# Optimization experiments

Hardware: AMD Instinct MI355X
Metric: run time of the kernel (lower is better)

Reference implementation:

```python
import jax, jax.numpy as jnp
import numpy as np

D_MODEL, D_K, D_V, D_H, SEQ = 1024, 64, 64, 16, 4096


def setup_inputs() -> dict:
    key = jax.random.key(0)
    ks = jax.random.split(key, 16)
    s = lambda fan_in: 1.0 / np.sqrt(fan_in)
    return {
        "X": jax.random.normal(ks[0], (SEQ, D_MODEL), jnp.float32),
        # shared Q/K/V projections (nn.Linear stores weight as [out, in])
        "Wq": jax.random.uniform(ks[1], (D_K, D_MODEL), jnp.float32, -s(D_MODEL), s(D_MODEL)),
        "bq": jax.random.uniform(ks[2], (D_K,), jnp.float32, -s(D_MODEL), s(D_MODEL)),
        "Wk": jax.random.uniform(ks[3], (D_K, D_MODEL), jnp.float32, -s(D_MODEL), s(D_MODEL)),
        "bk": jax.random.uniform(ks[4], (D_K,), jnp.float32, -s(D_MODEL), s(D_MODEL)),
        "Wv": jax.random.uniform(ks[5], (D_V, D_MODEL), jnp.float32, -s(D_MODEL), s(D_MODEL)),
        "bv": jax.random.uniform(ks[6], (D_V,), jnp.float32, -s(D_MODEL), s(D_MODEL)),
        # per-head linears stacked along head axis
        "Whq": jax.random.uniform(ks[7], (D_H, D_K, D_K), jnp.float32, -s(D_K), s(D_K)),
        "bhq": jax.random.uniform(ks[8], (D_H, D_K), jnp.float32, -s(D_K), s(D_K)),
        "Whk": jax.random.uniform(ks[9], (D_H, D_K, D_K), jnp.float32, -s(D_K), s(D_K)),
        "bhk": jax.random.uniform(ks[10], (D_H, D_K), jnp.float32, -s(D_K), s(D_K)),
        "Whv": jax.random.uniform(ks[11], (D_H, D_V, D_V), jnp.float32, -s(D_V), s(D_V)),
        "bhv": jax.random.uniform(ks[12], (D_H, D_V), jnp.float32, -s(D_V), s(D_V)),
        # final projection: d_h*d_v -> d_model
        "Wo": jax.random.uniform(ks[13], (D_MODEL, D_H * D_V), jnp.float32, -s(D_H * D_V), s(D_H * D_V)),
        "bo": jax.random.uniform(ks[14], (D_MODEL,), jnp.float32, -s(D_H * D_V), s(D_H * D_V)),
    }


def reference(X, Wq, bq, Wk, bk, Wv, bv, Whq, bhq, Whk, bhk, Whv, bhv, Wo, bo):
    # shared projections: [T, d_k] / [T, d_v]
    Q = X @ Wq.T + bq
    K = X @ Wk.T + bk
    V = X @ Wv.T + bv
    # per-head linears, all heads at once: [H, T, d_k]
    qh = jnp.einsum("tk,hjk->htj", Q, Whq) + bhq[:, None, :]
    kh = jnp.einsum("tk,hjk->htj", K, Whk) + bhk[:, None, :]
    vh = jnp.einsum("tv,hjv->htj", V, Whv) + bhv[:, None, :]
    # scaled dot-product attention per head: [H, T, T]
    scale = 1.0 / jnp.sqrt(jnp.asarray(Q.shape[-1], X.dtype))
    attn = jax.nn.softmax(jnp.einsum("htk,hsk->hts", qh, kh) * scale, axis=-1)
    rep = jnp.einsum("hts,hsv->htv", attn, vh)  # [H, T, d_v]
    # hstack heads -> [T, H*d_v], then final projection
    concat = rep.transpose(1, 0, 2).reshape(X.shape[0], -1)
    return concat @ Wo.T + bo
```

## Files before the change

### kernel.cpp

```cpp
#include <hip/hip_runtime.h>

#define T 4096
#define DM 1024
#define DK 64
#define H 16

typedef short s8 __attribute__((ext_vector_type(8)));
typedef float f4 __attribute__((ext_vector_type(4)));
typedef float f16v __attribute__((ext_vector_type(16)));
typedef unsigned short us4 __attribute__((ext_vector_type(4)));
typedef unsigned u32x2 __attribute__((ext_vector_type(2)));
typedef unsigned u32x4 __attribute__((ext_vector_type(4)));
typedef __bf16 bf2 __attribute__((ext_vector_type(2)));

#define MFMA16(a,b,c) __builtin_amdgcn_mfma_f32_16x16x32_bf16((a),(b),(c),0,0,0)
#define MFMA32(a,b,c) __builtin_amdgcn_mfma_f32_32x32x16_bf16((a),(b),(c),0,0,0)
#define SCALE_Q 0.18033688011112042f

__device__ __forceinline__ unsigned short f2bf(float x){
  __bf16 b = (__bf16)x;
  return __builtin_bit_cast(unsigned short, b);
}
__device__ __forceinline__ unsigned pk2(float a, float b){
  bf2 v; v[0] = (__bf16)a; v[1] = (__bf16)b;
  return __builtin_bit_cast(unsigned, v);
}

__device__ __forceinline__ void gload16(const void* g, void* lds){
  __builtin_amdgcn_global_load_lds((const __attribute__((address_space(1))) unsigned int*)g,
                                   (__attribute__((address_space(3))) unsigned int*)lds,
                                   16, 0, 0);
}

__device__ __forceinline__ void swp(unsigned X, unsigned Y, unsigned &E, unsigned &O){
#if __has_builtin(__builtin_amdgcn_permlane32_swap)
  auto a = __builtin_amdgcn_permlane32_swap(X, Y, false, false);
  E = a[0]; O = a[1];
#else
  int l = threadIdx.x & 63;
  unsigned sx = __builtin_amdgcn_ds_bpermute(((l & 31) << 2), X);
  unsigned sy = __builtin_amdgcn_ds_bpermute(((l & 31) << 2), Y);
  unsigned hx = __builtin_amdgcn_ds_bpermute((((l & 31) + 32) << 2), X);
  unsigned hy = __builtin_amdgcn_ds_bpermute((((l & 31) + 32) << 2), Y);
  E = (l < 32) ? sx : sy;
  O = (l < 32) ? hx : hy;
#endif
}

__global__ void cvt_bf16(const float* __restrict__ in, unsigned short* __restrict__ out, int n4){
  int i = blockIdx.x * blockDim.x + threadIdx.x;
  if (i >= n4) return;
  float4 v = reinterpret_cast<const float4*>(in)[i];
  us4 o;
  o[0] = f2bf(v.x); o[1] = f2bf(v.y); o[2] = f2bf(v.z); o[3] = f2bf(v.w);
  reinterpret_cast<us4*>(out)[i] = o;
}

#define N_WOB (DM * DM / 4)
#define N_W3  (64 * DM / 4)
#define N_WH  (16 * 64 * 64 / 4)
__global__ __launch_bounds__(256) void prep_all(
    const float* __restrict__ Wo,
    const float* __restrict__ Wq, const float* __restrict__ Wk, const float* __restrict__ Wv,
    const float* __restrict__ Whq, const float* __restrict__ Whk, const float* __restrict__ Whv,
    const float* __restrict__ bq, const float* __restrict__ bk, const float* __restrict__ bv,
    const float* __restrict__ bhq, const float* __restrict__ bhk, const float* __restrict__ bhv,
    unsigned short* __restrict__ Wob, unsigned short* __restrict__ W3b,
    unsigned short* __restrict__ Whb, float* __restrict__ beff){
  int idx = blockIdx.x * 256 + threadIdx.x;
  if (idx < N_WOB){
    float4 v = reinterpret_cast<const float4*>(Wo)[idx];
    us4 o; o[0]=f2bf(v.x); o[1]=f2bf(v.y); o[2]=f2bf(v.z); o[3]=f2bf(v.w);
    reinterpret_cast<us4*>(Wob)[idx] = o;
    return;
  }
  idx -= N_WOB;
  if (idx < 3 * N_W3){
    int seg = idx / N_W3, i = idx - seg * N_W3;
    const float* src = (seg == 0) ? Wq : ((seg == 1) ? Wk : Wv);
    float4 v = reinterpret_cast<const float4*>(src)[i];
    us4 o; o[0]=f2bf(v.x); o[1]=f2bf(v.y); o[2]=f2bf(v.z); o[3]=f2bf(v.w);
    reinterpret_cast<us4*>(W3b)[seg * N_W3 + i] = o;
    return;
  }
  idx -= 3 * N_W3;
  if (idx < 3 * N_WH){
    int seg = idx / N_WH, i = idx - seg * N_WH;
    const float* src = (seg == 0) ? Whq : ((seg == 1) ? Whk : Whv);
    float s = (seg == 0) ? SCALE_Q : 1.0f;
    float4 v = reinterpret_cast<const float4*>(src)[i];
    us4 o; o[0]=f2bf(v.x*s); o[1]=f2bf(v.y*s); o[2]=f2bf(v.z*s); o[3]=f2bf(v.w*s);
    reinterpret_cast<us4*>(Whb)[seg * N_WH + i] = o;
    return;
  }
  idx -= 3 * N_WH;
  if (idx < 3072){
    int seg = idx >> 10, j = idx & 1023;
    const float* Wh = (seg == 0) ? Whq : ((seg == 1) ? Whk : Whv);
    const float* b  = (seg == 0) ? bq  : ((seg == 1) ? bk  : bv);
    const float* bh = (seg == 0) ? bhq : ((seg == 1) ? bhk : bhv);
    float s = (seg == 0) ? SCALE_Q : 1.0f;
    const float* wr = Wh + j * 64;
    float acc = 0.f;
    #pragma unroll 8
    for (int k = 0; k < 64; ++k) acc += wr[k] * b[k];
    beff[idx] = (acc + bh[j]) * s;
  }
}

template<int MODE, int BM, int BN, int NT>
__global__ __launch_bounds__(256) void gemmX(const unsigned short* __restrict__ A,
                       const unsigned short* __restrict__ B,
                       const float* __restrict__ bias,
                       unsigned short* __restrict__ q_out,
                       unsigned short* __restrict__ k_out,
                       unsigned short* __restrict__ v_out,
                       float* __restrict__ f_out){
  __shared__ __align__(16) short la[2][BM * 64];
  __shared__ __align__(16) short lb[2][BN * 64];
  const int tid = threadIdx.x;
  const int wv = tid >> 6, l = tid & 63;
  const int lr = l & 15, lh = l >> 4;
  const int wr = wv >> 1, wc = wv & 1;
  const int tm = blockIdx.x / NT, tn = blockIdx.x % NT;
  const int t0 = tm * BM, o0 = tn * BN;
  constexpr int MF = BM / 32;
  constexpr int NF = BN / 32;
  constexpr int ACH = BM / 32;
  constexpr int BCH = BN / 32;
  constexpr int LAB = BM * 128;
  constexpr int LBB = BN * 128;

  f4 acc[MF][NF];
  #pragma unroll
  for (int i = 0; i < MF; ++i)
    #pragma unroll
    for (int j = 0; j < NF; ++j) acc[i][j] = (f4){0.f, 0.f, 0.f, 0.f};

  const int srow = tid >> 3;
  const int scs  = (tid & 7) ^ (srow & 7);
  const unsigned short* ap = A + (size_t)(t0 + srow) * DM + scs * 8;
  const unsigned short* bp = B + (size_t)(o0 + srow) * DM + scs * 8;
  char* ad = (char*)&la[0][0] + tid * 16;
  char* bd = (char*)&lb[0][0] + tid * 16;

  auto stage = [&](int BUF){
    #pragma unroll
    for (int i = 0; i < ACH; ++i)
      gload16(ap + (size_t)i * 32 * DM, ad + BUF * LAB + i * 4096);
    #pragma unroll
    for (int i = 0; i < BCH; ++i)
      gload16(bp + (size_t)i * 32 * DM, bd + BUF * LBB + i * 4096);
    ap += 64; bp += 64;
  };

  const int asw0 = (lh ^ (lr & 7)) * 16, asw1 = ((lh ^ 4) ^ (lr & 7)) * 16;
  const char* aB0 = (const char*)&la[0][0] + (wr * (BM / 2) + lr) * 128 + asw0;
  const char* aB1 = (const char*)&la[0][0] + (wr * (BM / 2) + lr) * 128 + asw1;
  const char* bB0 = (const char*)&lb[0][0] + (wc * (BN / 2) + lr) * 128 + asw0;
  const char* bB1 = (const char*)&lb[0][0] + (wc * (BN / 2) + lr) * 128 + asw1;

  auto step = [&](int BUF, bool dostage){
    if (dostage) stage(BUF ^ 1);
    s8 af[MF][2], bfr[NF][2];
    #pragma unroll
    for (int mf = 0; mf < MF; ++mf){
      af[mf][0] = *(const s8*)(aB0 + BUF * LAB + mf * 2048);
      af[mf][1] = *(const s8*)(aB1 + BUF * LAB + mf * 2048);
    }
    #pragma unroll
    for (int nf = 0; nf < NF; ++nf){
      bfr[nf][0] = *(const s8*)(bB0 + BUF * LBB + nf * 2048);
      bfr[nf][1] = *(const s8*)(bB1 + BUF * LBB + nf * 2048);
    }
    __builtin_amdgcn_s_setprio(1);
    #pragma unroll
    for (int mf = 0; mf < MF; ++mf)
      #pragma unroll
      for (int nf = 0; nf < NF; ++nf){
        acc[mf][nf] = MFMA16(af[mf][0], bfr[nf][0], acc[mf][nf]);
        acc[mf][nf] = MFMA16(af[mf][1], bfr[nf][1], acc[mf][nf]);
      }
    __builtin_amdgcn_s_setprio(0);
    __syncthreads();
  };

  stage(0);
  __syncthreads();
  #pragma unroll 1
  for (int t2 = 0; t2 < 8; ++t2){
    step(0, true);
    step(1, t2 < 7);
  }

  #pragma unroll
  for (int nf = 0; nf < NF; ++nf){
    int o = o0 + wc * (BN / 2) + nf * 16 + lr;
    float bs = (MODE == 4) ? 0.f : bias[o];
    int sel = o >> 6, oc = o & 63;
    unsigned short* yo = (sel == 0) ? q_out : ((sel == 1) ? k_out : v_out);
    #pragma unroll
    for (int mf = 0; mf < MF; ++mf)
      #pragma unroll
      for (int r = 0; r < 4; ++r){
        int t = t0 + wr * (BM / 2) + mf * 16 + lh * 4 + r;
        float v = acc[mf][nf][r] + bs;
        if (MODE == 2) f_out[(size_t)t * DM + o] = v;
        else           yo[(size_t)t * 64 + oc] = f2bf(v);
      }
  }
}

__global__ __launch_bounds__(256) void gemm_heads(const unsigned short* __restrict__ Yq,
                        const unsigned short* __restrict__ Yk,
                        const unsigned short* __restrict__ Yv,
                        const unsigned short* __restrict__ Whb,
                        const float* __restrict__ beff,
                        unsigned short* __restrict__ qhb,
                        unsigned short* __restrict__ khb,
                        unsigned short* __restrict__ vtb){
  const int tid = threadIdx.x;
  const int wv = tid >> 6, l = tid & 63;
  const int lr = l & 15, lh = l >> 4;
  const int rem = blockIdx.x % 48, tb = blockIdx.x / 48;
  const int kind = rem >> 4, h = rem & 15;
  const unsigned short* Y = (kind == 0) ? Yq : ((kind == 1) ? Yk : Yv);
  const unsigned short* B = Whb + (size_t)rem * 4096;
  const int t0 = tb * 256 + wv * 64;

  s8 wf[4][2], yf[4][2];
  #pragma unroll
  for (int nf = 0; nf < 4; ++nf)
    #pragma unroll
    for (int hf = 0; hf < 2; ++hf)
      wf[nf][hf] = *reinterpret_cast<const s8*>(B + (size_t)(nf * 16 + lr) * 64 + hf * 32 + lh * 8);
  #pragma unroll
  for (int mf = 0; mf < 4; ++mf)
    #pragma unroll
    for (int hf = 0; hf < 2; ++hf)
      yf[mf][hf] = *reinterpret_cast<const s8*>(Y + (size_t)(t0 + mf * 16 + lr) * 64 + hf * 32 + lh * 8);

  f4 acc[4][4];
  #pragma unroll
  for (int i = 0; i < 4; ++i)
    #pragma unroll
    for (int j = 0; j < 4; ++j) acc[i][j] = (f4){0.f, 0.f, 0.f, 0.f};

  if (kind < 2){
    #pragma unroll
    for (int mf = 0; mf < 4; ++mf)
      #pragma unroll
      for (int nf = 0; nf < 4; ++nf){
        acc[mf][nf] = MFMA16(yf[mf][0], wf[nf][0], acc[mf][nf]);
        acc[mf][nf] = MFMA16(yf[mf][1], wf[nf][1], acc[mf][nf]);
      }
    unsigned short* out = (kind == 0) ? qhb : khb;
    #pragma unroll
    for (int nf = 0; nf < 4; ++nf){
      int j = nf * 16 + lr;
      float bs = beff[rem * 64 + j];
      #pragma unroll
      for (int mf = 0; mf < 4; ++mf)
        #pragma unroll
        for (int r = 0; r < 4; ++r){
          int t = t0 + mf * 16 + lh * 4 + r;
          out[((size_t)h * T + t) * DK + j] = f2bf(acc[mf][nf][r] + bs);
        }
    }
  } else {
    #pragma unroll
    for (int nf = 0; nf < 4; ++nf)
      #pragma unroll
      for (int mf = 0; mf < 4; ++mf){
        acc[nf][mf] = MFMA16(wf[nf][0], yf[mf][0], acc[nf][mf]);
        acc[nf][mf] = MFMA16(wf[nf][1], yf[mf][1], acc[nf][mf]);
      }
    #pragma unroll
    for (int nf = 0; nf < 4; ++nf){
      float4 bsv = *reinterpret_cast<const float4*>(beff + rem * 64 + nf * 16 + lh * 4);
      #pragma unroll
      for (int r = 0; r < 4; ++r){
        int j = nf * 16 + lh * 4 + r;
        float bs = (r == 0) ? bsv.x : ((r == 1) ? bsv.y : ((r == 2) ? bsv.z : bsv.w));
        #pragma unroll
        for (int mf = 0; mf < 4; ++mf){
          int t = t0 + mf * 16 + lr;
          vtb[((size_t)h * DK + j) * T + t] = f2bf(acc[nf][mf][r] + bs);
        }
      }
    }
  }
}

__global__ __launch_bounds__(256) void attn_fwd(const unsigned short* __restrict__ qh,
                         const unsigned short* __restrict__ kh,
                         const unsigned short* __restrict__ vt,
                         unsigned short* __restrict__ cat){
  __shared__ __align__(16) char ldsb[2][16384];
  const int tid = threadIdx.x;
  const int wv = tid >> 6, l = tid & 63;
  const int l31 = l & 31, h5 = l >> 5, l7 = l & 7;
  const int h = blockIdx.x >> 5, qblk = blockIdx.x & 31;
  const int Q0w = qblk * 128 + wv * 32;

  s8 qf[4];
  #pragma unroll
  for (int kk = 0; kk < 4; ++kk)
    qf[kk] = *reinterpret_cast<const s8*>(
        qh + ((size_t)h * T + Q0w + l31) * DK + kk * 16 + h5 * 8);

  float ls = 0.f;
  f16v oa0, oa1;
  #pragma unroll
  for (int i = 0; i < 16; ++i){ oa0[i] = 0.f; oa1[i] = 0.f; }

  const int srow = tid >> 3;
  const int scs  = (tid & 7) ^ (srow & 7);
  const unsigned short* kp = kh + (size_t)h * T * DK + srow * DK + scs * 8;
  const unsigned short* vp = vt + (size_t)h * DK * T + srow * T + scs * 8;
  char* sd = &ldsb[0][0] + tid * 16;

  auto stage = [&](int BUF){
    gload16(kp,           sd + BUF * 16384);
    gload16(kp + 32 * DK, sd + BUF * 16384 + 4096);
    gload16(vp,           sd + BUF * 16384 + 8192);
    gload16(vp + 32 * T,  sd + BUF * 16384 + 12288);
    kp += 64 * DK; vp += 64;
  };

  const char* ba[2][4];
  #pragma unroll
  for (int t2 = 0; t2 < 2; ++t2)
    #pragma unroll
    for (int kk = 0; kk < 4; ++kk)
      ba[t2][kk] = &ldsb[0][0] + (t2 * 32 + l31) * 128 + ((((kk << 1) | h5) ^ l7) << 4);

  auto step = [&](int BUF, bool dostage){
    if (dostage) stage(BUF ^ 1);
    s8 kf0[4], kf1[4];
    #pragma unroll
    for (int kk = 0; kk < 4; ++kk){
      kf0[kk] = *(const s8*)(ba[0][kk] + BUF * 16384);
      kf1[kk] = *(const s8*)(ba[1][kk] + BUF * 16384);
    }
    f16v sc0, sc1;
    #pragma unroll
    for (int i = 0; i < 16; ++i){ sc0[i] = 0.f; sc1[i] = 0.f; }
    __builtin_amdgcn_s_setprio(1);
    #pragma unroll
    for (int kk = 0; kk < 4; ++kk) sc0 = MFMA32(kf0[kk], qf[kk], sc0);
    #pragma unroll
    for (int kk = 0; kk < 4; ++kk) sc1 = MFMA32(kf1[kk], qf[kk], sc1);
    __builtin_amdgcn_s_setprio(0);
    s8 vf0[4], vf1[4];
    #pragma unroll
    for (int p = 0; p < 4; ++p){
      vf0[p] = *(const s8*)(ba[0][p] + BUF * 16384 + 8192);
      vf1[p] = *(const s8*)(ba[1][p] + BUF * 16384 + 8192);
    }
    float p0[16], p1[16];
    #pragma unroll
    for (int i = 0; i < 16; ++i){
      p0[i] = __builtin_amdgcn_exp2f(sc0[i]);
      p1[i] = __builtin_amdgcn_exp2f(sc1[i]);
    }
    float r0 = (p0[0]+p0[1]) + (p0[2]+p0[3]);
    float r1 = (p0[4]+p0[5]) + (p0[6]+p0[7]);
    float r2 = (p0[8]+p0[9]) + (p0[10]+p0[11]);
    float r3 = (p0[12]+p0[13]) + (p0[14]+p0[15]);
    float r4 = (p1[0]+p1[1]) + (p1[2]+p1[3]);
    float r5 = (p1[4]+p1[5]) + (p1[6]+p1[7]);
    float r6 = (p1[8]+p1[9]) + (p1[10]+p1[11]);
    float r7 = (p1[12]+p1[13]) + (p1[14]+p1[15]);
    ls += ((r0+r1)+(r2+r3)) + ((r4+r5)+(r6+r7));
    unsigned a0 = pk2(p0[0],p0[1]),  a1 = pk2(p0[2],p0[3]);
    unsigned a2 = pk2(p0[4],p0[5]),  a3 = pk2(p0[6],p0[7]);
    unsigned a4 = pk2(p0[8],p0[9]),  a5 = pk2(p0[10],p0[11]);
    unsigned a6 = pk2(p0[12],p0[13]), a7 = pk2(p0[14],p0[15]);
    unsigned b0 = pk2(p1[0],p1[1]),  b1 = pk2(p1[2],p1[3]);
    unsigned b2 = pk2(p1[4],p1[5]),  b3 = pk2(p1[6],p1[7]);
    unsigned b4 = pk2(p1[8],p1[9]),  b5 = pk2(p1[10],p1[11]);
    unsigned b6 = pk2(p1[12],p1[13]), b7 = pk2(p1[14],p1[15]);
    unsigned e0,o0, e1,o1, e2,o2, e3,o3, e4,o4, e5,o5, e6,o6, e7,o7;
    swp(a0, a2, e0, o0);  swp(a1, a3, e1, o1);
    swp(a4, a6, e2, o2);  swp(a5, a7, e3, o3);
    swp(b0, b2, e4, o4);  swp(b1, b3, e5, o5);
    swp(b4, b6, e6, o6);  swp(b5, b7, e7, o7);
    u32x4 pu0 = {e0, e1, o0, o1};
    u32x4 pu1 = {e2, e3, o2, o3};
    u32x4 pu2 = {e4, e5, o4, o5};
    u32x4 pu3 = {e6, e7, o6, o7};
    s8 pa0 = __builtin_bit_cast(s8, pu0);
    s8 pa1 = __builtin_bit_cast(s8, pu1);
    s8 pa2 = __builtin_bit_cast(s8, pu2);
    s8 pa3 = __builtin_bit_cast(s8, pu3);
    __builtin_amdgcn_s_setprio(1);
    oa0 = MFMA32(vf0[0], pa0, oa0);
    oa0 = MFMA32(vf0[1], pa1, oa0);
    oa0 = MFMA32(vf0[2], pa2, oa0);
    oa0 = MFMA32(vf0[3], pa3, oa0);
    oa1 = MFMA32(vf1[0], pa0, oa1);
    oa1 = MFMA32(vf1[1], pa1, oa1);
    oa1 = MFMA32(vf1[2], pa2, oa1);
    oa1 = MFMA32(vf1[3], pa3, oa1);
    __builtin_amdgcn_s_setprio(0);
    __syncthreads();
  };

  stage(0);
  __syncthreads();
  #pragma unroll 1
  for (int it = 0; it < 32; ++it){
    step(0, true);
    step(1, it < 31);
  }

  float lq = ls + __shfl_xor(ls, 32);
  float inv = 1.f / lq;
  const int t = Q0w + l31;
  unsigned short* crow = cat + (size_t)t * DM + h * DK;
  #pragma unroll
  for (int g = 0; g < 4; ++g){
    u32x2 w0, w1;
    w0[0] = pk2(oa0[g*4+0] * inv, oa0[g*4+1] * inv);
    w0[1] = pk2(oa0[g*4+2] * inv, oa0[g*4+3] * inv);
    w1[0] = pk2(oa1[g*4+0] * inv, oa1[g*4+1] * inv);
    w1[1] = pk2(oa1[g*4+2] * inv, oa1[g*4+3] * inv);
    *reinterpret_cast<u32x2*>(crow + g * 8 + h5 * 4)      = w0;
    *reinterpret_cast<u32x2*>(crow + 32 + g * 8 + h5 * 4) = w1;
  }
}

extern "C" void kernel_launch(void* const* d_in, const int* in_sizes, int n_in,
                              void* d_out, int out_size, void* d_ws, size_t ws_size,
                              hipStream_t stream){
  const float* X   = (const float*)d_in[0];
  const float* Wq  = (const float*)d_in[1];
  const float* bq  = (const float*)d_in[2];
  const float* Wk  = (const float*)d_in[3];
  const float* bk  = (const float*)d_in[4];
  const float* Wv  = (const float*)d_in[5];
  const float* bv  = (const float*)d_in[6];
  const float* Whq = (const float*)d_in[7];
  const float* bhq = (const float*)d_in[8];
  const float* Whk = (const float*)d_in[9];
  const float* bhk = (const float*)d_in[10];
  const float* Whv = (const float*)d_in[11];
  const float* bhv = (const float*)d_in[12];
  const float* Wo  = (const float*)d_in[13];
  const float* bo  = (const float*)d_in[14];

  char* w = (char*)d_ws;
  size_t off = 0;
  auto alloc = [&](size_t bytes) -> char* {
    char* p = w + off;
    off = (off + bytes + 255) & ~(size_t)255;
    return p;
  };
  unsigned short* Xbf = (unsigned short*)alloc((size_t)T * DM * 2);
  unsigned short* Wob = (unsigned short*)alloc((size_t)DM * DM * 2);
  unsigned short* W3b = (unsigned short*)alloc((size_t)192 * DM * 2);
  unsigned short* Whb = (unsigned short*)alloc((size_t)48 * 64 * 64 * 2);
  float* beff = (float*)alloc(48 * 64 * 4);
  unsigned short* Yq  = (unsigned short*)alloc((size_t)T * 64 * 2);
  unsigned short* Yk  = (unsigned short*)alloc((size_t)T * 64 * 2);
  unsigned short* Yv  = (unsigned short*)alloc((size_t)T * 64 * 2);
  unsigned short* qhb = (unsigned short*)alloc((size_t)H * T * DK * 2);
  unsigned short* khb = (unsigned short*)alloc((size_t)H * T * DK * 2);
  unsigned short* vtb = (unsigned short*)alloc((size_t)H * T * DK * 2);
  unsigned short* cat = Xbf;

  cvt_bf16<<<(T * DM / 4) / 256, 256, 0, stream>>>(X, Xbf, T * DM / 4);
  {
    int total = N_WOB + 3 * N_W3 + 3 * N_WH + 3072;
    prep_all<<<(total + 255) / 256, 256, 0, stream>>>(
        Wo, Wq, Wk, Wv, Whq, Whk, Whv, bq, bk, bv, bhq, bhk, bhv,
        Wob, W3b, Whb, beff);
  }

  gemmX<4, 64, 64, 3><<<(T / 64) * 3, 256, 0, stream>>>(Xbf, W3b, nullptr, Yq, Yk, Yv, nullptr);

  gemm_heads<<<(T / 256) * 48, 256, 0, stream>>>(Yq, Yk, Yv, Whb, beff, qhb, khb, vtb);

  attn_fwd<<<(T / 128) * H, 256, 0, stream>>>(qhb, khb, vtb, cat);

  gemmX<2, 128, 64, 16><<<(T / 128) * 16, 256, 0, stream>>>(cat, Wob, bo, nullptr, nullptr, nullptr, (float*)d_out);
}
```

Baseline: 143.4 us.

## Process two 32-row query tiles per wave in attention with 2-wave blocks

The attention kernel now runs 128-thread blocks where each wave handles 64 query rows as two 32-row tiles, reusing each K/V fragment loaded from LDS for both tiles. This halves LDS fragment reads per unit of MFMA work, and the staging loop is restructured so 128 threads still fill the same 16KB K/V buffer. The cost is doubled accumulator and query registers per wave, which may lower occupancy, and fewer waves per block to hide latency.

```diff
diff --git a/kernel.cpp b/kernel.cpp
--- a/kernel.cpp
+++ b/kernel.cpp
@@ -292,7 +292,7 @@
   }
 }
 
-__global__ __launch_bounds__(256) void attn_fwd(const unsigned short* __restrict__ qh,
+__global__ __launch_bounds__(128) void attn_fwd(const unsigned short* __restrict__ qh,
                          const unsigned short* __restrict__ kh,
                          const unsigned short* __restrict__ vt,
                          unsigned short* __restrict__ cat){
@@ -301,18 +301,24 @@
   const int wv = tid >> 6, l = tid & 63;
   const int l31 = l & 31, h5 = l >> 5, l7 = l & 7;
   const int h = blockIdx.x >> 5, qblk = blockIdx.x & 31;
-  const int Q0w = qblk * 128 + wv * 32;
-
-  s8 qf[4];
-  #pragma unroll
-  for (int kk = 0; kk < 4; ++kk)
-    qf[kk] = *reinterpret_cast<const s8*>(
-        qh + ((size_t)h * T + Q0w + l31) * DK + kk * 16 + h5 * 8);
-
-  float ls = 0.f;
-  f16v oa0, oa1;
-  #pragma unroll
-  for (int i = 0; i < 16; ++i){ oa0[i] = 0.f; oa1[i] = 0.f; }
+  const int Qw = qblk * 128 + wv * 64;
+
+  s8 qf[2][4];
+  #pragma unroll
+  for (int qt = 0; qt < 2; ++qt)
+    #pragma unroll
+    for (int kk = 0; kk < 4; ++kk)
+      qf[qt][kk] = *reinterpret_cast<const s8*>(
+          qh + ((size_t)h * T + Qw + qt * 32 + l31) * DK + kk * 16 + h5 * 8);
+
+  float ls[2] = {0.f, 0.f};
+  f16v oa[2][2];
+  #pragma unroll
+  for (int qt = 0; qt < 2; ++qt)
+    #pragma unroll
+    for (int dt = 0; dt < 2; ++dt)
+      #pragma unroll
+      for (int i = 0; i < 16; ++i) oa[qt][dt][i] = 0.f;
 
   const int srow = tid >> 3;
   const int scs  = (tid & 7) ^ (srow & 7);
@@ -321,89 +327,92 @@
   char* sd = &ldsb[0][0] + tid * 16;
 
   auto stage = [&](int BUF){
-    gload16(kp,           sd + BUF * 16384);
-    gload16(kp + 32 * DK, sd + BUF * 16384 + 4096);
-    gload16(vp,           sd + BUF * 16384 + 8192);
-    gload16(vp + 32 * T,  sd + BUF * 16384 + 12288);
+    #pragma unroll
+    for (int i = 0; i < 4; ++i)
+      gload16(kp + (size_t)i * 16 * DK, sd + BUF * 16384 + i * 2048);
+    #pragma unroll
+    for (int i = 0; i < 4; ++i)
+      gload16(vp + (size_t)i * 16 * T, sd + BUF * 16384 + 8192 + i * 2048);
     kp += 64 * DK; vp += 64;
   };
 
-  const char* ba[2][4];
-  #pragma unroll
-  for (int t2 = 0; t2 < 2; ++t2)
-    #pragma unroll
-    for (int kk = 0; kk < 4; ++kk)
-      ba[t2][kk] = &ldsb[0][0] + (t2 * 32 + l31) * 128 + ((((kk << 1) | h5) ^ l7) << 4);
+  const char* ba[4];
+  #pragma unroll
+  for (int kk = 0; kk < 4; ++kk)
+    ba[kk] = &ldsb[0][0] + l31 * 128 + ((((kk << 1) | h5) ^ l7) << 4);
 
   auto step = [&](int BUF, bool dostage){
     if (dostage) stage(BUF ^ 1);
-    s8 kf0[4], kf1[4];
+    const int bo = BUF * 16384;
+    s8 kf0[4], kf1[4], vf0[4], vf1[4];
     #pragma unroll
     for (int kk = 0; kk < 4; ++kk){
-      kf0[kk] = *(const s8*)(ba[0][kk] + BUF * 16384);
-      kf1[kk] = *(const s8*)(ba[1][kk] + BUF * 16384);
-    }
-    f16v sc0, sc1;
-    #pragma unroll
-    for (int i = 0; i < 16; ++i){ sc0[i] = 0.f; sc1[i] = 0.f; }
-    __builtin_amdgcn_s_setprio(1);
-    #pragma unroll
-    for (int kk = 0; kk < 4; ++kk) sc0 = MFMA32(kf0[kk], qf[kk], sc0);
-    #pragma unroll
-    for (int kk = 0; kk < 4; ++kk) sc1 = MFMA32(kf1[kk], qf[kk], sc1);
-    __builtin_amdgcn_s_setprio(0);
-    s8 vf0[4], vf1[4];
+      kf0[kk] = *(const s8*)(ba[kk] + bo);
+      kf1[kk] = *(const s8*)(ba[kk] + bo + 4096);
+    }
     #pragma unroll
     for (int p = 0; p < 4; ++p){
-      vf0[p] = *(const s8*)(ba[0][p] + BUF * 16384 + 8192);
-      vf1[p] = *(const s8*)(ba[1][p] + BUF * 16384 + 8192);
-    }
-    float p0[16], p1[16];
-    #pragma unroll
-    for (int i = 0; i < 16; ++i){
-      p0[i] = __builtin_amdgcn_exp2f(sc0[i]);
-      p1[i] = __builtin_amdgcn_exp2f(sc1[i]);
-    }
-    float r0 = (p0[0]+p0[1]) + (p0[2]+p0[3]);
-    float r1 = (p0[4]+p0[5]) + (p0[6]+p0[7]);
-    float r2 = (p0[8]+p0[9]) + (p0[10]+p0[11]);
-    float r3 = (p0[12]+p0[13]) + (p0[14]+p0[15]);
-    float r4 = (p1[0]+p1[1]) + (p1[2]+p1[3]);
-    float r5 = (p1[4]+p1[5]) + (p1[6]+p1[7]);
-    float r6 = (p1[8]+p1[9]) + (p1[10]+p1[11]);
-    float r7 = (p1[12]+p1[13]) + (p1[14]+p1[15]);
-    ls += ((r0+r1)+(r2+r3)) + ((r4+r5)+(r6+r7));
-    unsigned a0 = pk2(p0[0],p0[1]),  a1 = pk2(p0[2],p0[3]);
-    unsigned a2 = pk2(p0[4],p0[5]),  a3 = pk2(p0[6],p0[7]);
-    unsigned a4 = pk2(p0[8],p0[9]),  a5 = pk2(p0[10],p0[11]);
-    unsigned a6 = pk2(p0[12],p0[13]), a7 = pk2(p0[14],p0[15]);
-    unsigned b0 = pk2(p1[0],p1[1]),  b1 = pk2(p1[2],p1[3]);
-    unsigned b2 = pk2(p1[4],p1[5]),  b3 = pk2(p1[6],p1[7]);
-    unsigned b4 = pk2(p1[8],p1[9]),  b5 = pk2(p1[10],p1[11]);
-    unsigned b6 = pk2(p1[12],p1[13]), b7 = pk2(p1[14],p1[15]);
-    unsigned e0,o0, e1,o1, e2,o2, e3,o3, e4,o4, e5,o5, e6,o6, e7,o7;
-    swp(a0, a2, e0, o0);  swp(a1, a3, e1, o1);
-    swp(a4, a6, e2, o2);  swp(a5, a7, e3, o3);
-    swp(b0, b2, e4, o4);  swp(b1, b3, e5, o5);
-    swp(b4, b6, e6, o6);  swp(b5, b7, e7, o7);
-    u32x4 pu0 = {e0, e1, o0, o1};
-    u32x4 pu1 = {e2, e3, o2, o3};
-    u32x4 pu2 = {e4, e5, o4, o5};
-    u32x4 pu3 = {e6, e7, o6, o7};
-    s8 pa0 = __builtin_bit_cast(s8, pu0);
-    s8 pa1 = __builtin_bit_cast(s8, pu1);
-    s8 pa2 = __builtin_bit_cast(s8, pu2);
-    s8 pa3 = __builtin_bit_cast(s8, pu3);
-    __builtin_amdgcn_s_setprio(1);
-    oa0 = MFMA32(vf0[0], pa0, oa0);
-    oa0 = MFMA32(vf0[1], pa1, oa0);
-    oa0 = MFMA32(vf0[2], pa2, oa0);
-    oa0 = MFMA32(vf0[3], pa3, oa0);
-    oa1 = MFMA32(vf1[0], pa0, oa1);
-    oa1 = MFMA32(vf1[1], pa1, oa1);
-    oa1 = MFMA32(vf1[2], pa2, oa1);
-    oa1 = MFMA32(vf1[3], pa3, oa1);
-    __builtin_amdgcn_s_setprio(0);
+      vf0[p] = *(const s8*)(ba[p] + bo + 8192);
+      vf1[p] = *(const s8*)(ba[p] + bo + 12288);
+    }
+    #pragma unroll
+    for (int qt = 0; qt < 2; ++qt){
+      f16v sc0, sc1;
+      #pragma unroll
+      for (int i = 0; i < 16; ++i){ sc0[i] = 0.f; sc1[i] = 0.f; }
+      __builtin_amdgcn_s_setprio(1);
+      #pragma unroll
+      for (int kk = 0; kk < 4; ++kk) sc0 = MFMA32(kf0[kk], qf[qt][kk], sc0);
+      #pragma unroll
+      for (int kk = 0; kk < 4; ++kk) sc1 = MFMA32(kf1[kk], qf[qt][kk], sc1);
+      __builtin_amdgcn_s_setprio(0);
+      float p0[16], p1[16];
+      #pragma unroll
+      for (int i = 0; i < 16; ++i){
+        p0[i] = __builtin_amdgcn_exp2f(sc0[i]);
+        p1[i] = __builtin_amdgcn_exp2f(sc1[i]);
+      }
+      float r0 = (p0[0]+p0[1]) + (p0[2]+p0[3]);
+      float r1 = (p0[4]+p0[5]) + (p0[6]+p0[7]);
+      float r2 = (p0[8]+p0[9]) + (p0[10]+p0[11]);
+      float r3 = (p0[12]+p0[13]) + (p0[14]+p0[15]);
+      float r4 = (p1[0]+p1[1]) + (p1[2]+p1[3]);
+      float r5 = (p1[4]+p1[5]) + (p1[6]+p1[7]);
+      float r6 = (p1[8]+p1[9]) + (p1[10]+p1[11]);
+      float r7 = (p1[12]+p1[13]) + (p1[14]+p1[15]);
+      ls[qt] += ((r0+r1)+(r2+r3)) + ((r4+r5)+(r6+r7));
+      unsigned a0 = pk2(p0[0],p0[1]),  a1 = pk2(p0[2],p0[3]);
+      unsigned a2 = pk2(p0[4],p0[5]),  a3 = pk2(p0[6],p0[7]);
+      unsigned a4 = pk2(p0[8],p0[9]),  a5 = pk2(p0[10],p0[11]);
+      unsigned a6 = pk2(p0[12],p0[13]), a7 = pk2(p0[14],p0[15]);
+      unsigned b0 = pk2(p1[0],p1[1]),  b1 = pk2(p1[2],p1[3]);
+      unsigned b2 = pk2(p1[4],p1[5]),  b3 = pk2(p1[6],p1[7]);
+      unsigned b4 = pk2(p1[8],p1[9]),  b5 = pk2(p1[10],p1[11]);
+      unsigned b6 = pk2(p1[12],p1[13]), b7 = pk2(p1[14],p1[15]);
+      unsigned e0,o0, e1,o1, e2,o2, e3,o3, e4,o4, e5,o5, e6,o6, e7,o7;
+      swp(a0, a2, e0, o0);  swp(a1, a3, e1, o1);
+      swp(a4, a6, e2, o2);  swp(a5, a7, e3, o3);
+      swp(b0, b2, e4, o4);  swp(b1, b3, e5, o5);
+      swp(b4, b6, e6, o6);  swp(b5, b7, e7, o7);
+      u32x4 pu0 = {e0, e1, o0, o1};
+      u32x4 pu1 = {e2, e3, o2, o3};
+      u32x4 pu2 = {e4, e5, o4, o5};
+      u32x4 pu3 = {e6, e7, o6, o7};
+      s8 pa0 = __builtin_bit_cast(s8, pu0);
+      s8 pa1 = __builtin_bit_cast(s8, pu1);
+      s8 pa2 = __builtin_bit_cast(s8, pu2);
+      s8 pa3 = __builtin_bit_cast(s8, pu3);
+      __builtin_amdgcn_s_setprio(1);
+      oa[qt][0] = MFMA32(vf0[0], pa0, oa[qt][0]);
+      oa[qt][0] = MFMA32(vf0[1], pa1, oa[qt][0]);
+      oa[qt][0] = MFMA32(vf0[2], pa2, oa[qt][0]);
+      oa[qt][0] = MFMA32(vf0[3], pa3, oa[qt][0]);
+      oa[qt][1] = MFMA32(vf1[0], pa0, oa[qt][1]);
+      oa[qt][1] = MFMA32(vf1[1], pa1, oa[qt][1]);
+      oa[qt][1] = MFMA32(vf1[2], pa2, oa[qt][1]);
+      oa[qt][1] = MFMA32(vf1[3], pa3, oa[qt][1]);
+      __builtin_amdgcn_s_setprio(0);
+    }
     __syncthreads();
   };
 
@@ -415,19 +424,22 @@
     step(1, it < 31);
   }
 
-  float lq = ls + __shfl_xor(ls, 32);
-  float inv = 1.f / lq;
-  const int t = Q0w + l31;
-  unsigned short* crow = cat + (size_t)t * DM + h * DK;
-  #pragma unroll
-  for (int g = 0; g < 4; ++g){
-    u32x2 w0, w1;
-    w0[0] = pk2(oa0[g*4+0] * inv, oa0[g*4+1] * inv);
-    w0[1] = pk2(oa0[g*4+2] * inv, oa0[g*4+3] * inv);
-    w1[0] = pk2(oa1[g*4+0] * inv, oa1[g*4+1] * inv);
-    w1[1] = pk2(oa1[g*4+2] * inv, oa1[g*4+3] * inv);
-    *reinterpret_cast<u32x2*>(crow + g * 8 + h5 * 4)      = w0;
-    *reinterpret_cast<u32x2*>(crow + 32 + g * 8 + h5 * 4) = w1;
+  #pragma unroll
+  for (int qt = 0; qt < 2; ++qt){
+    float lq = ls[qt] + __shfl_xor(ls[qt], 32);
+    float inv = 1.f / lq;
+    const int t = Qw + qt * 32 + l31;
+    unsigned short* crow = cat + (size_t)t * DM + h * DK;
+    #pragma unroll
+    for (int g = 0; g < 4; ++g){
+      u32x2 w0, w1;
+      w0[0] = pk2(oa[qt][0][g*4+0] * inv, oa[qt][0][g*4+1] * inv);
+      w0[1] = pk2(oa[qt][0][g*4+2] * inv, oa[qt][0][g*4+3] * inv);
+      w1[0] = pk2(oa[qt][1][g*4+0] * inv, oa[qt][1][g*4+1] * inv);
+      w1[1] = pk2(oa[qt][1][g*4+2] * inv, oa[qt][1][g*4+3] * inv);
+      *reinterpret_cast<u32x2*>(crow + g * 8 + h5 * 4)      = w0;
+      *reinterpret_cast<u32x2*>(crow + 32 + g * 8 + h5 * 4) = w1;
+    }
   }
 }
 
@@ -482,7 +494,7 @@
 
   gemm_heads<<<(T / 256) * 48, 256, 0, stream>>>(Yq, Yk, Yv, Whb, beff, qhb, khb, vtb);
 
-  attn_fwd<<<(T / 128) * H, 256, 0, stream>>>(qhb, khb, vtb, cat);
+  attn_fwd<<<(T / 128) * H, 128, 0, stream>>>(qhb, khb, vtb, cat);
 
   gemmX<2, 128, 64, 16><<<(T / 128) * 16, 256, 0, stream>>>(cat, Wob, bo, nullptr, nullptr, nullptr, (float*)d_out);
 }
```

Result: no change. 142.9 us (-0.4%).

## Triple-buffer K/V tiles and software-pipeline QK^T one tile ahead of softmax/PV

Applied to the files above, without the earlier changes.

Moves the attention loop from double to triple LDS buffering, prefetching two tiles ahead. It also computes the QK^T scores for the next tile before doing exp and the PV MFMAs for the current tile, so score MFMAs can overlap the softmax VALU work. This costs more LDS per block (48KB), which may lower occupancy, and more registers to hold the extra score accumulators.

```diff
diff --git a/kernel.cpp b/kernel.cpp
--- a/kernel.cpp
+++ b/kernel.cpp
@@ -296,7 +296,7 @@
                          const unsigned short* __restrict__ kh,
                          const unsigned short* __restrict__ vt,
                          unsigned short* __restrict__ cat){
-  __shared__ __align__(16) char ldsb[2][16384];
+  __shared__ __align__(16) char ldsb[3][16384];
   const int tid = threadIdx.x;
   const int wv = tid >> 6, l = tid & 63;
   const int l31 = l & 31, h5 = l >> 5, l7 = l & 7;
@@ -320,11 +320,11 @@
   const unsigned short* vp = vt + (size_t)h * DK * T + srow * T + scs * 8;
   char* sd = &ldsb[0][0] + tid * 16;
 
-  auto stage = [&](int BUF){
-    gload16(kp,           sd + BUF * 16384);
-    gload16(kp + 32 * DK, sd + BUF * 16384 + 4096);
-    gload16(vp,           sd + BUF * 16384 + 8192);
-    gload16(vp + 32 * T,  sd + BUF * 16384 + 12288);
+  auto stage = [&](int BOFF){
+    gload16(kp,           sd + BOFF);
+    gload16(kp + 32 * DK, sd + BOFF + 4096);
+    gload16(vp,           sd + BOFF + 8192);
+    gload16(vp + 32 * T,  sd + BOFF + 12288);
     kp += 64 * DK; vp += 64;
   };
 
@@ -335,34 +335,54 @@
     for (int kk = 0; kk < 4; ++kk)
       ba[t2][kk] = &ldsb[0][0] + (t2 * 32 + l31) * 128 + ((((kk << 1) | h5) ^ l7) << 4);
 
-  auto step = [&](int BUF, bool dostage){
-    if (dostage) stage(BUF ^ 1);
+  stage(0);
+  stage(16384);
+  __syncthreads();
+
+  f16v scA0, scA1;
+  {
     s8 kf0[4], kf1[4];
     #pragma unroll
     for (int kk = 0; kk < 4; ++kk){
-      kf0[kk] = *(const s8*)(ba[0][kk] + BUF * 16384);
-      kf1[kk] = *(const s8*)(ba[1][kk] + BUF * 16384);
-    }
-    f16v sc0, sc1;
-    #pragma unroll
-    for (int i = 0; i < 16; ++i){ sc0[i] = 0.f; sc1[i] = 0.f; }
-    __builtin_amdgcn_s_setprio(1);
-    #pragma unroll
-    for (int kk = 0; kk < 4; ++kk) sc0 = MFMA32(kf0[kk], qf[kk], sc0);
-    #pragma unroll
-    for (int kk = 0; kk < 4; ++kk) sc1 = MFMA32(kf1[kk], qf[kk], sc1);
-    __builtin_amdgcn_s_setprio(0);
-    s8 vf0[4], vf1[4];
-    #pragma unroll
-    for (int p = 0; p < 4; ++p){
-      vf0[p] = *(const s8*)(ba[0][p] + BUF * 16384 + 8192);
-      vf1[p] = *(const s8*)(ba[1][p] + BUF * 16384 + 8192);
-    }
+      kf0[kk] = *(const s8*)(ba[0][kk]);
+      kf1[kk] = *(const s8*)(ba[1][kk]);
+    }
+    #pragma unroll
+    for (int i = 0; i < 16; ++i){ scA0[i] = 0.f; scA1[i] = 0.f; }
+    #pragma unroll
+    for (int kk = 0; kk < 4; ++kk) scA0 = MFMA32(kf0[kk], qf[kk], scA0);
+    #pragma unroll
+    for (int kk = 0; kk < 4; ++kk) scA1 = MFMA32(kf1[kk], qf[kk], scA1);
+  }
+
+  int curOff = 0, nxtOff = 16384, filOff = 32768;
+  #pragma unroll 1
+  for (int it = 0; it < 64; ++it){
+    if (it < 62) stage(filOff);
+
+    f16v scB0, scB1;
+    if (it < 63){
+      s8 kf0[4], kf1[4];
+      #pragma unroll
+      for (int kk = 0; kk < 4; ++kk){
+        kf0[kk] = *(const s8*)(ba[0][kk] + nxtOff);
+        kf1[kk] = *(const s8*)(ba[1][kk] + nxtOff);
+      }
+      #pragma unroll
+      for (int i = 0; i < 16; ++i){ scB0[i] = 0.f; scB1[i] = 0.f; }
+      __builtin_amdgcn_s_setprio(1);
+      #pragma unroll
+      for (int kk = 0; kk < 4; ++kk) scB0 = MFMA32(kf0[kk], qf[kk], scB0);
+      #pragma unroll
+      for (int kk = 0; kk < 4; ++kk) scB1 = MFMA32(kf1[kk], qf[kk], scB1);
+      __builtin_amdgcn_s_setprio(0);
+    }
+
     float p0[16], p1[16];
     #pragma unroll
     for (int i = 0; i < 16; ++i){
-      p0[i] = __builtin_amdgcn_exp2f(sc0[i]);
-      p1[i] = __builtin_amdgcn_exp2f(sc1[i]);
+      p0[i] = __builtin_amdgcn_exp2f(scA0[i]);
+      p1[i] = __builtin_amdgcn_exp2f(scA1[i]);
     }
     float r0 = (p0[0]+p0[1]) + (p0[2]+p0[3]);
     float r1 = (p0[4]+p0[5]) + (p0[6]+p0[7]);
@@ -394,6 +414,13 @@
     s8 pa1 = __builtin_bit_cast(s8, pu1);
     s8 pa2 = __builtin_bit_cast(s8, pu2);
     s8 pa3 = __builtin_bit_cast(s8, pu3);
+
+    s8 vf0[4], vf1[4];
+    #pragma unroll
+    for (int p = 0; p < 4; ++p){
+      vf0[p] = *(const s8*)(ba[0][p] + curOff + 8192);
+      vf1[p] = *(const s8*)(ba[1][p] + curOff + 8192);
+    }
     __builtin_amdgcn_s_setprio(1);
     oa0 = MFMA32(vf0[0], pa0, oa0);
     oa0 = MFMA32(vf0[1], pa1, oa0);
@@ -404,15 +431,10 @@
     oa1 = MFMA32(vf1[2], pa2, oa1);
     oa1 = MFMA32(vf1[3], pa3, oa1);
     __builtin_amdgcn_s_setprio(0);
+
+    if (it < 63){ scA0 = scB0; scA1 = scB1; }
+    int tmp = curOff; curOff = nxtOff; nxtOff = filOff; filOff = tmp;
     __syncthreads();
-  };
-
-  stage(0);
-  __syncthreads();
-  #pragma unroll 1
-  for (int it = 0; it < 32; ++it){
-    step(0, true);
-    step(1, it < 31);
   }
 
   float lq = ls + __shfl_xor(ls, 32);
```

New measurement: 142.0 us, median of 2. Within noise of the previous version (-1.0%).

## Double attention KV stage size per barrier and fold X conversion into prep kernel

Applied to the files above, without the earlier changes.

The attention kernel now stages 128 keys and values per buffer instead of 64, with 32 KB per buffer. Each loop iteration processes two 64-key subtiles and hits one barrier where there were two, which halves synchronisation and issues larger prefetches. The price is doubled LDS use (64 KB per block), which may lower occupancy. Separately, the X-to-bf16 conversion is merged into the prep_all kernel, removing one kernel launch.

```diff
diff --git a/kernel.cpp b/kernel.cpp
--- a/kernel.cpp
+++ b/kernel.cpp
@@ -47,27 +47,27 @@
 #endif
 }
 
-__global__ void cvt_bf16(const float* __restrict__ in, unsigned short* __restrict__ out, int n4){
-  int i = blockIdx.x * blockDim.x + threadIdx.x;
-  if (i >= n4) return;
-  float4 v = reinterpret_cast<const float4*>(in)[i];
-  us4 o;
-  o[0] = f2bf(v.x); o[1] = f2bf(v.y); o[2] = f2bf(v.z); o[3] = f2bf(v.w);
-  reinterpret_cast<us4*>(out)[i] = o;
-}
-
+#define N_X   (T * DM / 4)
 #define N_WOB (DM * DM / 4)
 #define N_W3  (64 * DM / 4)
 #define N_WH  (16 * 64 * 64 / 4)
 __global__ __launch_bounds__(256) void prep_all(
-    const float* __restrict__ Wo,
+    const float* __restrict__ X, const float* __restrict__ Wo,
     const float* __restrict__ Wq, const float* __restrict__ Wk, const float* __restrict__ Wv,
     const float* __restrict__ Whq, const float* __restrict__ Whk, const float* __restrict__ Whv,
     const float* __restrict__ bq, const float* __restrict__ bk, const float* __restrict__ bv,
     const float* __restrict__ bhq, const float* __restrict__ bhk, const float* __restrict__ bhv,
-    unsigned short* __restrict__ Wob, unsigned short* __restrict__ W3b,
-    unsigned short* __restrict__ Whb, float* __restrict__ beff){
+    unsigned short* __restrict__ Xbf, unsigned short* __restrict__ Wob,
+    unsigned short* __restrict__ W3b, unsigned short* __restrict__ Whb,
+    float* __restrict__ beff){
   int idx = blockIdx.x * 256 + threadIdx.x;
+  if (idx < N_X){
+    float4 v = reinterpret_cast<const float4*>(X)[idx];
+    us4 o; o[0]=f2bf(v.x); o[1]=f2bf(v.y); o[2]=f2bf(v.z); o[3]=f2bf(v.w);
+    reinterpret_cast<us4*>(Xbf)[idx] = o;
+    return;
+  }
+  idx -= N_X;
   if (idx < N_WOB){
     float4 v = reinterpret_cast<const float4*>(Wo)[idx];
     us4 o; o[0]=f2bf(v.x); o[1]=f2bf(v.y); o[2]=f2bf(v.z); o[3]=f2bf(v.w);
@@ -296,7 +296,7 @@
                          const unsigned short* __restrict__ kh,
                          const unsigned short* __restrict__ vt,
                          unsigned short* __restrict__ cat){
-  __shared__ __align__(16) char ldsb[2][16384];
+  __shared__ __align__(16) char ldsb[2][32768];
   const int tid = threadIdx.x;
   const int wv = tid >> 6, l = tid & 63;
   const int l31 = l & 31, h5 = l >> 5, l7 = l & 7;
@@ -321,11 +321,16 @@
   char* sd = &ldsb[0][0] + tid * 16;
 
   auto stage = [&](int BUF){
-    gload16(kp,           sd + BUF * 16384);
-    gload16(kp + 32 * DK, sd + BUF * 16384 + 4096);
-    gload16(vp,           sd + BUF * 16384 + 8192);
-    gload16(vp + 32 * T,  sd + BUF * 16384 + 12288);
-    kp += 64 * DK; vp += 64;
+    const int b = BUF * 32768;
+    gload16(kp,            sd + b);
+    gload16(kp + 32 * DK,  sd + b + 4096);
+    gload16(vp,            sd + b + 8192);
+    gload16(vp + 32 * T,   sd + b + 12288);
+    gload16(kp + 64 * DK,  sd + b + 16384);
+    gload16(kp + 96 * DK,  sd + b + 20480);
+    gload16(vp + 64,       sd + b + 24576);
+    gload16(vp + 32 * T + 64, sd + b + 28672);
+    kp += 128 * DK; vp += 128;
   };
 
   const char* ba[2][4];
@@ -335,13 +340,12 @@
     for (int kk = 0; kk < 4; ++kk)
       ba[t2][kk] = &ldsb[0][0] + (t2 * 32 + l31) * 128 + ((((kk << 1) | h5) ^ l7) << 4);
 
-  auto step = [&](int BUF, bool dostage){
-    if (dostage) stage(BUF ^ 1);
+  auto subtile = [&](int boff){
     s8 kf0[4], kf1[4];
     #pragma unroll
     for (int kk = 0; kk < 4; ++kk){
-      kf0[kk] = *(const s8*)(ba[0][kk] + BUF * 16384);
-      kf1[kk] = *(const s8*)(ba[1][kk] + BUF * 16384);
+      kf0[kk] = *(const s8*)(ba[0][kk] + boff);
+      kf1[kk] = *(const s8*)(ba[1][kk] + boff);
     }
     f16v sc0, sc1;
     #pragma unroll
@@ -355,8 +359,8 @@
     s8 vf0[4], vf1[4];
     #pragma unroll
     for (int p = 0; p < 4; ++p){
-      vf0[p] = *(const s8*)(ba[0][p] + BUF * 16384 + 8192);
-      vf1[p] = *(const s8*)(ba[1][p] + BUF * 16384 + 8192);
+      vf0[p] = *(const s8*)(ba[0][p] + boff + 8192);
+      vf1[p] = *(const s8*)(ba[1][p] + boff + 8192);
     }
     float p0[16], p1[16];
     #pragma unroll
@@ -404,15 +408,17 @@
     oa1 = MFMA32(vf1[2], pa2, oa1);
     oa1 = MFMA32(vf1[3], pa3, oa1);
     __builtin_amdgcn_s_setprio(0);
-    __syncthreads();
   };
 
   stage(0);
   __syncthreads();
   #pragma unroll 1
   for (int it = 0; it < 32; ++it){
-    step(0, true);
-    step(1, it < 31);
+    const int BUF = it & 1;
+    if (it < 31) stage(BUF ^ 1);
+    subtile(BUF * 32768);
+    subtile(BUF * 32768 + 16384);
+    __syncthreads();
   }
 
   float lq = ls + __shfl_xor(ls, 32);
@@ -470,12 +476,11 @@
   unsigned short* vtb = (unsigned short*)alloc((size_t)H * T * DK * 2);
   unsigned short* cat = Xbf;
 
-  cvt_bf16<<<(T * DM / 4) / 256, 256, 0, stream>>>(X, Xbf, T * DM / 4);
   {
-    int total = N_WOB + 3 * N_W3 + 3 * N_WH + 3072;
+    int total = N_X + N_WOB + 3 * N_W3 + 3 * N_WH + 3072;
     prep_all<<<(total + 255) / 256, 256, 0, stream>>>(
-        Wo, Wq, Wk, Wv, Whq, Whk, Whv, bq, bk, bv, bhq, bhk, bhv,
-        Wob, W3b, Whb, beff);
+        X, Wo, Wq, Wk, Wv, Whq, Whk, Whv, bq, bk, bv, bhq, bhk, bhv,
+        Xbf, Wob, W3b, Whb, beff);
   }
 
   gemmX<4, 64, 64, 3><<<(T / 64) * 3, 256, 0, stream>>>(Xbf, W3b, nullptr, Yq, Yk, Yv, nullptr);
```

New measurement: 142.9 us. No clear change (-0.4%).
